# Optimization experiments

Hardware: AMD Instinct MI355X
Metric: run time of the kernel (lower is better)

The kernel has to match this reference:

```python
import jax, jax.numpy as jnp
import numpy as np

B, N, C, H = 8, 2048, 2048, 16


def setup_inputs() -> dict:
    key = jax.random.key(0)
    k1, k2, k3, k4 = jax.random.split(key, 4)
    x = jax.random.normal(k1, (B, N, C), dtype=jnp.float32)
    W_attn = jax.random.normal(k2, (C, C), dtype=jnp.float32) * 0.02
    W_proj = jax.random.normal(k3, (C, C), dtype=jnp.float32) * 0.02
    temp = jnp.ones((H, 1), dtype=jnp.float32)
    denom_bias = jax.random.normal(k4, (H, N, 1), dtype=jnp.float32) * 0.01
    return {"x": x, "W_attn": W_attn, "W_proj": W_proj, "temp": temp, "denom_bias": denom_bias}


def reference(x, W_attn, W_proj, temp, denom_bias):
    # x: (B, N, C); dropout layers are identity in eval mode.
    b, n, c = x.shape
    h = temp.shape[0]
    d = c // h
    eps = jnp.float32(jnp.finfo(jnp.float16).eps)  # fp16 eps used by the original

    # w: (B, H, N, D)
    w = jnp.einsum('bnc,oc->bno', x, W_attn).reshape(b, n, h, d).transpose(0, 2, 1, 3)
    w_sq = w * w

    # cumulative per-feature normalization along sequence
    denom = jnp.maximum(jnp.cumsum(w_sq, axis=2), eps)              # (B,H,N,D)
    w_normed = w_sq / denom + denom_bias[None, :, :n, :]            # (B,H,N,D)

    tmp = jnp.sum(w_normed, axis=-1) * temp[None]                   # (B,H,N), temp (H,1) broadcasts over N
    Pi = jax.nn.softmax(tmp, axis=1)                                # softmax over heads

    # second cumulative scan weighted by Pi
    dots = jnp.cumsum(w_sq * Pi[..., None], axis=2) / (jnp.cumsum(Pi, axis=-1) + eps)[..., None]
    attn = 1.0 / (1.0 + dots)                                       # (B,H,N,D)

    y = -(w * Pi[..., None]) * attn                                 # (B,H,N,D)
    y = y.transpose(0, 2, 1, 3).reshape(b, n, c)                    # (B,N,C)
    return jnp.einsum('bnc,oc->bno', y, W_proj)
```

## Files before the change

### kernel.cpp

```cpp
#include <hip/hip_runtime.h>
#include <math.h>

typedef _Float16 f16;
typedef f16 f16x8 __attribute__((ext_vector_type(8)));
typedef float f32x4 __attribute__((ext_vector_type(4)));

#define EPS_F16 0.0009765625f


__global__ __launch_bounds__(256) void k_cast8h(const float* __restrict__ in,
                                                f16* __restrict__ out,
                                                long long n8) {
  long long i = (long long)blockIdx.x * blockDim.x + threadIdx.x;
  if (i >= n8) return;
  const float4* in4 = (const float4*)in;
  float4 a = in4[i * 2];
  float4 b = in4[i * 2 + 1];
  f16x8 o;
  o[0] = (f16)a.x; o[1] = (f16)a.y; o[2] = (f16)a.z; o[3] = (f16)a.w;
  o[4] = (f16)b.x; o[5] = (f16)b.y; o[6] = (f16)b.z; o[7] = (f16)b.w;
  *(f16x8*)(out + i * 8) = o;
}

__device__ __forceinline__ void gl2lds16(const void* g, void* l) {
  __builtin_amdgcn_global_load_lds(
      (const __attribute__((address_space(1))) void*)g,
      (__attribute__((address_space(3))) void*)l, 16, 0, 0);
}

__device__ __forceinline__ void drain_barrier() {
  asm volatile("s_waitcnt vmcnt(0) lgkmcnt(0)" ::: "memory");
  __builtin_amdgcn_sched_barrier(0);
  __syncthreads();
}

template <int MODE>
__global__ __launch_bounds__(512, 2) void gemm256(const f16* __restrict__ A,
                                                  const f16* __restrict__ Bm,
                                                  float* __restrict__ Cout,
                                                  f16* __restrict__ Wout,
                                                  float* __restrict__ psum) {
  constexpr int K = 2048;
  __shared__ alignas(16) char lds[131072];
  const int t = threadIdx.x;
  const int lane = t & 63;
  const int wid = t >> 6;
  const int wm = wid >> 2;
  const int wn = wid & 3;

  const int lin = blockIdx.y * 8 + blockIdx.x;
  const int logical = (lin & 7) * 64 + (lin >> 3);
  const size_t bm = (size_t)(logical >> 3) * 256;
  const size_t bn = (size_t)(logical & 7) * 256;

  size_t aOff[4], bOff[4];
  int sp[4];
#pragma unroll
  for (int j = 0; j < 4; ++j) {
    int sr = j * 64 + (t >> 7) * 16 + ((t & 63) >> 2);
    int sc = ((t >> 6) & 1) * 32 + (((t & 3) * 8) ^ (((t >> 5) & 1) << 4));
    sp[j] = j * 8192 + t * 16;
    aOff[j] = (bm + (size_t)sr) * K + sc;
    bOff[j] = (bn + (size_t)sr) * K + sc;
  }

  const int lbyte = (((lane & 15) * 64 + (lane >> 4) * 16) ^ ((lane & 8) << 2));

  f32x4 acc[8][4] = {};

#pragma unroll
  for (int j = 0; j < 4; ++j) {
    gl2lds16(A + aOff[j], lds + sp[j]);
    gl2lds16(Bm + bOff[j], lds + 32768 + sp[j]);
  }
  drain_barrier();

  int s = 0;
  for (int kt = 0; kt < K / 64; ++kt) {
    if (kt + 1 < K / 64) {
      const int ns = s ^ 1;
      const size_t ko = (size_t)(kt + 1) * 64;
#pragma unroll
      for (int j = 0; j < 4; ++j) {
        gl2lds16(A + aOff[j] + ko, lds + ns * 65536 + sp[j]);
        gl2lds16(Bm + bOff[j] + ko, lds + ns * 65536 + 32768 + sp[j]);
      }
    }
    const char* Ab = lds + s * 65536 + wm * 16384 + lbyte;
    const char* Bb = lds + s * 65536 + 32768 + wn * 8192 + lbyte;
    f16x8 bfrag[4][2];
#pragma unroll
    for (int q = 0; q < 4; ++q) {
      if (q == 0) {
#pragma unroll
        for (int fj = 0; fj < 4; ++fj)
#pragma unroll
          for (int k2 = 0; k2 < 2; ++k2)
            bfrag[fj][k2] = *(const f16x8*)(Bb + (fj * 2 + k2) * 1024);
      }
      f16x8 afrag[2][2];
#pragma unroll
      for (int mi = 0; mi < 2; ++mi)
#pragma unroll
        for (int k2 = 0; k2 < 2; ++k2)
          afrag[mi][k2] = *(const f16x8*)(Ab + ((q * 2 + mi) * 2 + k2) * 1024);
#pragma unroll
      for (int mi = 0; mi < 2; ++mi)
#pragma unroll
        for (int fj = 0; fj < 4; ++fj)
#pragma unroll
          for (int k2 = 0; k2 < 2; ++k2)
            acc[q * 2 + mi][fj] = __builtin_amdgcn_mfma_f32_16x16x32_f16(
                afrag[mi][k2], bfrag[fj][k2], acc[q * 2 + mi][fj], 0, 0, 0);
    }
    drain_barrier();
    s ^= 1;
  }

  const int col = lane & 15;
  const int rb = (lane >> 4) * 4;
  if constexpr (MODE == 0) {
#pragma unroll
    for (int fi = 0; fi < 8; ++fi)
#pragma unroll
      for (int fj = 0; fj < 4; ++fj)
#pragma unroll
        for (int r = 0; r < 4; ++r) {
          size_t gr = bm + wm * 128 + fi * 16 + rb + r;
          size_t gc = bn + wn * 64 + fj * 16 + col;
          Cout[gr * 2048 + gc] = acc[fi][fj][r];
        }
  } else {
#pragma unroll
    for (int fj = 0; fj < 4; ++fj) {
      float ss = 0.f;
#pragma unroll
      for (int fi = 0; fi < 8; ++fi)
#pragma unroll
        for (int r = 0; r < 4; ++r) {
          size_t gr = bm + wm * 128 + fi * 16 + rb + r;
          size_t gc = bn + wn * 64 + fj * 16 + col;
          f16 q = (f16)acc[fi][fj][r];
          Wout[(((gr >> 11) * 16 + (gc >> 7)) * 2048 + (gr & 2047)) * 128 +
               (gc & 127)] = q;
          float qf = (float)q;
          ss += qf * qf;
        }
      ss += __shfl_xor(ss, 16);
      ss += __shfl_xor(ss, 32);
      if (lane < 16) {
        int b = (int)(bm >> 11);
        int h = (int)(bn >> 7) + (wn >> 1);
        int chunk = (int)((bm & 2047) >> 7) + wm;
        int d = (wn & 1) * 64 + fj * 16 + lane;
        psum[(((size_t)(b * 16 + h)) * 16 + chunk) * 128 + d] = ss;
      }
    }
  }
}

__global__ __launch_bounds__(256) void k_prefix(float* __restrict__ psum) {
  int idx = blockIdx.x * 256 + threadIdx.x;
  int bh = idx >> 7, d = idx & 127;
  float run = 0.f;
#pragma unroll
  for (int c = 0; c < 16; ++c) {
    size_t o = ((size_t)bh * 16 + c) * 128 + d;
    float v = psum[o];
    psum[o] = run;
    run += v;
  }
}

__device__ __forceinline__ int swz(int i, int j) { return i * 128 + (j ^ (i & 31)); }

__global__ __launch_bounds__(128) void k_tmp(const f16* __restrict__ w,
                                             const float* __restrict__ pre,
                                             const float* __restrict__ dbias,
                                             const float* __restrict__ temp,
                                             float* __restrict__ tmp) {
  __shared__ float ratio[128 * 128];
  int blk = blockIdx.x;
  int bh = blk >> 4, chunk = blk & 15;
  int h = bh & 15;
  int d = threadIdx.x;
  const f16* base =
      w + ((size_t)bh * 2048 + (size_t)chunk * 128) * 128 + d;
  float cum = pre[((size_t)bh * 16 + chunk) * 128 + d];
  for (int i = 0; i < 128; ++i) {
    float v = (float)base[(size_t)i * 128];
    float sq = v * v;
    cum += sq;
    float dn = fmaxf(cum, EPS_F16);
    ratio[swz(i, d)] = sq / dn;
  }
  __syncthreads();
  float s = 0.f;
#pragma unroll 8
  for (int j = 0; j < 128; ++j) s += ratio[swz(d, j)];
  int n = chunk * 128 + d;
  tmp[(size_t)bh * 2048 + n] = (s + 128.f * dbias[h * 2048 + n]) * temp[h];
}

__global__ __launch_bounds__(256) void k_softmax(const float* __restrict__ tmp,
                                                 float* __restrict__ Pi) {
  int idx = blockIdx.x * 256 + threadIdx.x;
  int b = idx >> 11, n = idx & 2047;
  float v[16];
  float mx = -1e30f;
#pragma unroll
  for (int h = 0; h < 16; ++h) {
    v[h] = tmp[((size_t)(b * 16 + h)) * 2048 + n];
    mx = fmaxf(mx, v[h]);
  }
  float s = 0.f;
#pragma unroll
  for (int h = 0; h < 16; ++h) {
    v[h] = expf(v[h] - mx);
    s += v[h];
  }
  float inv = 1.f / s;
#pragma unroll
  for (int h = 0; h < 16; ++h)
    Pi[((size_t)(b * 16 + h)) * 2048 + n] = v[h] * inv;
}

__global__ __launch_bounds__(128) void k_partial2(const f16* __restrict__ w,
                                                  const float* __restrict__ Pi,
                                                  float* __restrict__ psum,
                                                  float* __restrict__ pisum) {
  int blk = blockIdx.x;
  int bh = blk >> 4, chunk = blk & 15;
  int d = threadIdx.x;
  const f16* base =
      w + ((size_t)bh * 2048 + (size_t)chunk * 128) * 128 + d;
  const float* pib = Pi + (size_t)bh * 2048 + (size_t)chunk * 128;
  float s = 0.f, sp = 0.f;
#pragma unroll 4
  for (int i = 0; i < 128; ++i) {
    float p = pib[i];
    float v = (float)base[(size_t)i * 128];
    s += v * v * p;
    sp += p;
  }
  psum[(size_t)blk * 128 + d] = s;
  if (d == 0) pisum[blk] = sp;
}

__global__ __launch_bounds__(128) void k_prefix_pi(float* __restrict__ pisum) {
  int bh = threadIdx.x;
  float run = 0.f;
#pragma unroll
  for (int c = 0; c < 16; ++c) {
    int o = bh * 16 + c;
    float v = pisum[o];
    pisum[o] = run;
    run += v;
  }
}

__global__ __launch_bounds__(128) void k_y(const f16* __restrict__ w,
                                           const float* __restrict__ Pi,
                                           const float* __restrict__ pre2,
                                           const float* __restrict__ piPre,
                                           f16* __restrict__ yout) {
  int blk = blockIdx.x;
  int bh = blk >> 4, chunk = blk & 15;
  int b = bh >> 4, h = bh & 15;
  int d = threadIdx.x;
  const f16* base =
      w + ((size_t)bh * 2048 + (size_t)chunk * 128) * 128 + d;
  const float* pib = Pi + (size_t)bh * 2048 + (size_t)chunk * 128;
  float cum = pre2[((size_t)bh * 16 + chunk) * 128 + d];
  float cpi = piPre[bh * 16 + chunk];
  for (int i = 0; i < 128; ++i) {
    float p = pib[i];
    float v = (float)base[(size_t)i * 128];
    cum += v * v * p;
    cpi += p;
    float dots = cum / (cpi + EPS_F16);
    float attn = 1.f / (1.f + dots);
    float y = -(v * p) * attn;
    int n = chunk * 128 + i;
    yout[((size_t)(b * 2048 + n)) * 2048 + h * 128 + d] = (f16)y;
  }
}

extern "C" void kernel_launch(void* const* d_in, const int* in_sizes, int n_in,
                              void* d_out, int out_size, void* d_ws, size_t ws_size,
                              hipStream_t stream) {
  const float* x     = (const float*)d_in[0];
  const float* Wa    = (const float*)d_in[1];
  const float* Wp    = (const float*)d_in[2];
  const float* temp  = (const float*)d_in[3];
  const float* dbias = (const float*)d_in[4];
  float* out = (float*)d_out;

  char* ws = (char*)d_ws;
  constexpr size_t OFF_W   = 0;
  constexpr size_t OFF_XH  = 67108864;
  constexpr size_t OFF_WAH = OFF_XH + 67108864;
  constexpr size_t OFF_WPB = OFF_WAH + 8388608;
  constexpr size_t OFF_TMP = OFF_WPB + 8388608;
  constexpr size_t OFF_PI  = OFF_TMP + 2097152;
  constexpr size_t OFF_PS  = OFF_PI + 2097152;
  constexpr size_t OFF_PIS = OFF_PS + 1048576;

  f16*   w    = (f16*)(ws + OFF_W);
  f16*   xh   = (f16*)(ws + OFF_XH);
  f16*   Wah  = (f16*)(ws + OFF_WAH);
  f16*   Wpb  = (f16*)(ws + OFF_WPB);
  float* tmp  = (float*)(ws + OFF_TMP);
  float* Pi   = (float*)(ws + OFF_PI);
  float* psum = (float*)(ws + OFF_PS);
  float* pis  = (float*)(ws + OFF_PIS);

  k_cast8h<<<16384, 256, 0, stream>>>(x, xh, 4194304LL);
  k_cast8h<<<2048, 256, 0, stream>>>(Wa, Wah, 524288LL);
  k_cast8h<<<2048, 256, 0, stream>>>(Wp, Wpb, 524288LL);

  gemm256<1><<<dim3(8, 64), 512, 0, stream>>>(xh, Wah, nullptr, w, psum);

  k_prefix<<<64, 256, 0, stream>>>(psum);
  k_tmp<<<2048, 128, 0, stream>>>(w, psum, dbias, temp, tmp);

  k_softmax<<<64, 256, 0, stream>>>(tmp, Pi);

  k_partial2<<<2048, 128, 0, stream>>>(w, Pi, psum, pis);
  k_prefix<<<64, 256, 0, stream>>>(psum);
  k_prefix_pi<<<1, 128, 0, stream>>>(pis);
  k_y<<<2048, 128, 0, stream>>>(w, Pi, psum, pis, xh);

  gemm256<0><<<dim3(8, 64), 512, 0, stream>>>(xh, Wpb, out, nullptr, nullptr);
}
```

Before: 445.5 us.

## Deepen GEMM LDS pipeline to four stages and stage W epilogue through LDS

```diff
diff --git a/kernel.cpp b/kernel.cpp
--- a/kernel.cpp
+++ b/kernel.cpp
@@ -28,10 +28,20 @@
       (__attribute__((address_space(3))) void*)l, 16, 0, 0);
 }
 
-__device__ __forceinline__ void drain_barrier() {
-  asm volatile("s_waitcnt vmcnt(0) lgkmcnt(0)" ::: "memory");
+template <int VM>
+__device__ __forceinline__ void wait_vm() {
+  if constexpr (VM == 8)      asm volatile("s_waitcnt vmcnt(8)" ::: "memory");
+  else if constexpr (VM == 4) asm volatile("s_waitcnt vmcnt(4)" ::: "memory");
+  else                        asm volatile("s_waitcnt vmcnt(0)" ::: "memory");
   __builtin_amdgcn_sched_barrier(0);
-  __syncthreads();
+}
+
+__device__ __forceinline__ void pipe_barrier() {
+  __builtin_amdgcn_sched_barrier(0);
+  asm volatile("" ::: "memory");
+  __builtin_amdgcn_s_barrier();
+  asm volatile("" ::: "memory");
+  __builtin_amdgcn_sched_barrier(0);
 }
 
 template <int MODE>
@@ -41,6 +51,7 @@
                                                   f16* __restrict__ Wout,
                                                   float* __restrict__ psum) {
   constexpr int K = 2048;
+  constexpr int NT = K / 32;
   __shared__ alignas(16) char lds[131072];
   const int t = threadIdx.x;
   const int lane = t & 63;
@@ -53,69 +64,67 @@
   const size_t bm = (size_t)(logical >> 3) * 256;
   const size_t bn = (size_t)(logical & 7) * 256;
 
-  size_t aOff[4], bOff[4];
-  int sp[4];
-#pragma unroll
-  for (int j = 0; j < 4; ++j) {
-    int sr = j * 64 + (t >> 7) * 16 + ((t & 63) >> 2);
-    int sc = ((t >> 6) & 1) * 32 + (((t & 3) * 8) ^ (((t >> 5) & 1) << 4));
-    sp[j] = j * 8192 + t * 16;
-    aOff[j] = (bm + (size_t)sr) * K + sc;
-    bOff[j] = (bn + (size_t)sr) * K + sc;
-  }
+  const int sk = ((t & 3) * 8) ^ (((t >> 5) & 1) << 4);
+  size_t aOff[2], bOff[2];
+#pragma unroll
+  for (int j = 0; j < 2; ++j) {
+    int sr = j * 128 + (t >> 6) * 16 + ((t & 63) >> 2);
+    aOff[j] = (bm + (size_t)sr) * K + sk;
+    bOff[j] = (bn + (size_t)sr) * K + sk;
+  }
+  const int t16 = t * 16;
 
   const int lbyte = (((lane & 15) * 64 + (lane >> 4) * 16) ^ ((lane & 8) << 2));
 
   f32x4 acc[8][4] = {};
 
-#pragma unroll
-  for (int j = 0; j < 4; ++j) {
-    gl2lds16(A + aOff[j], lds + sp[j]);
-    gl2lds16(Bm + bOff[j], lds + 32768 + sp[j]);
-  }
-  drain_barrier();
-
-  int s = 0;
-  for (int kt = 0; kt < K / 64; ++kt) {
-    if (kt + 1 < K / 64) {
-      const int ns = s ^ 1;
-      const size_t ko = (size_t)(kt + 1) * 64;
-#pragma unroll
-      for (int j = 0; j < 4; ++j) {
-        gl2lds16(A + aOff[j] + ko, lds + ns * 65536 + sp[j]);
-        gl2lds16(Bm + bOff[j] + ko, lds + ns * 65536 + 32768 + sp[j]);
+  auto stage_tile = [&](int kt) {
+    char* base = lds + (kt & 3) * 32768;
+    const size_t ko = (size_t)kt * 32;
+#pragma unroll
+    for (int j = 0; j < 2; ++j) {
+      gl2lds16(A + aOff[j] + ko, base + j * 8192 + t16);
+      gl2lds16(Bm + bOff[j] + ko, base + 16384 + j * 8192 + t16);
+    }
+  };
+
+  auto compute_tile = [&](int slot) {
+    const char* Ab = lds + slot * 32768 + wm * 8192 + lbyte;
+    const char* Bb = lds + slot * 32768 + 16384 + wn * 4096 + lbyte;
+    f16x8 bfr[4];
+#pragma unroll
+    for (int fj = 0; fj < 4; ++fj) bfr[fj] = *(const f16x8*)(Bb + fj * 1024);
+#pragma unroll
+    for (int q = 0; q < 4; ++q) {
+      f16x8 af0 = *(const f16x8*)(Ab + (q * 2) * 1024);
+      f16x8 af1 = *(const f16x8*)(Ab + (q * 2 + 1) * 1024);
+      __builtin_amdgcn_s_setprio(1);
+#pragma unroll
+      for (int fj = 0; fj < 4; ++fj) {
+        acc[q * 2][fj] = __builtin_amdgcn_mfma_f32_16x16x32_f16(
+            af0, bfr[fj], acc[q * 2][fj], 0, 0, 0);
+        acc[q * 2 + 1][fj] = __builtin_amdgcn_mfma_f32_16x16x32_f16(
+            af1, bfr[fj], acc[q * 2 + 1][fj], 0, 0, 0);
       }
+      __builtin_amdgcn_s_setprio(0);
     }
-    const char* Ab = lds + s * 65536 + wm * 16384 + lbyte;
-    const char* Bb = lds + s * 65536 + 32768 + wn * 8192 + lbyte;
-    f16x8 bfrag[4][2];
-#pragma unroll
-    for (int q = 0; q < 4; ++q) {
-      if (q == 0) {
-#pragma unroll
-        for (int fj = 0; fj < 4; ++fj)
-#pragma unroll
-          for (int k2 = 0; k2 < 2; ++k2)
-            bfrag[fj][k2] = *(const f16x8*)(Bb + (fj * 2 + k2) * 1024);
-      }
-      f16x8 afrag[2][2];
-#pragma unroll
-      for (int mi = 0; mi < 2; ++mi)
-#pragma unroll
-        for (int k2 = 0; k2 < 2; ++k2)
-          afrag[mi][k2] = *(const f16x8*)(Ab + ((q * 2 + mi) * 2 + k2) * 1024);
-#pragma unroll
-      for (int mi = 0; mi < 2; ++mi)
-#pragma unroll
-        for (int fj = 0; fj < 4; ++fj)
-#pragma unroll
-          for (int k2 = 0; k2 < 2; ++k2)
-            acc[q * 2 + mi][fj] = __builtin_amdgcn_mfma_f32_16x16x32_f16(
-                afrag[mi][k2], bfrag[fj][k2], acc[q * 2 + mi][fj], 0, 0, 0);
-    }
-    drain_barrier();
-    s ^= 1;
-  }
+  };
+
+  stage_tile(0);
+  stage_tile(1);
+  stage_tile(2);
+  wait_vm<8>();
+  pipe_barrier();
+
+  for (int kt = 0; kt <= NT - 4; ++kt) {
+    stage_tile(kt + 3);
+    compute_tile(kt & 3);
+    wait_vm<8>();
+    pipe_barrier();
+  }
+  compute_tile((NT - 3) & 3); wait_vm<4>(); pipe_barrier();
+  compute_tile((NT - 2) & 3); wait_vm<0>(); pipe_barrier();
+  compute_tile((NT - 1) & 3); pipe_barrier();
 
   const int col = lane & 15;
   const int rb = (lane >> 4) * 4;
@@ -131,6 +140,7 @@
           Cout[gr * 2048 + gc] = acc[fi][fj][r];
         }
   } else {
+    char* W = lds + wid * 16384;
 #pragma unroll
     for (int fj = 0; fj < 4; ++fj) {
       float ss = 0.f;
@@ -138,11 +148,11 @@
       for (int fi = 0; fi < 8; ++fi)
 #pragma unroll
         for (int r = 0; r < 4; ++r) {
-          size_t gr = bm + wm * 128 + fi * 16 + rb + r;
-          size_t gc = bn + wn * 64 + fj * 16 + col;
+          int row_l = fi * 16 + rb + r;
+          int d_l = fj * 16 + col;
           f16 q = (f16)acc[fi][fj][r];
-          Wout[(((gr >> 11) * 16 + (gc >> 7)) * 2048 + (gr & 2047)) * 128 +
-               (gc & 127)] = q;
+          *(f16*)(W + row_l * 128 +
+                  ((d_l * 2) ^ (((row_l >> 2) & 3) << 5))) = q;
           float qf = (float)q;
           ss += qf * qf;
         }
@@ -155,6 +165,20 @@
         int d = (wn & 1) * 64 + fj * 16 + lane;
         psum[(((size_t)(b * 16 + h)) * 16 + chunk) * 128 + d] = ss;
       }
+    }
+    asm volatile("s_waitcnt lgkmcnt(0)" ::: "memory");
+    __builtin_amdgcn_sched_barrier(0);
+#pragma unroll
+    for (int it = 0; it < 16; ++it) {
+      int row_l = it * 8 + (lane >> 3);
+      int g2 = (row_l >> 2) & 3;
+      int c_p = lane & 7;
+      f16x8 v = *(const f16x8*)(W + row_l * 128 + ((c_p * 16) ^ (g2 << 5)));
+      size_t gr = bm + wm * 128 + row_l;
+      int h = (int)(bn >> 7) + (wn >> 1);
+      int d = (wn & 1) * 64 + c_p * 8;
+      *(f16x8*)(Wout + (((gr >> 11) * 16 + h) * 2048 + (gr & 2047)) * 128 + d) =
+          v;
     }
   }
 }
```

After: 440.2 us. Within noise of the previous version (-1.2%).
